# Optimization experiments

Measured on AMD Instinct MI355X. Metric: run time of the kernel, lower is better.

The kernel has to match this reference:

```python
import jax, jax.numpy as jnp
import numpy as np

N_EMBD = 1024
N_HEAD = 16
HEAD_DIM = N_EMBD // N_HEAD
SCALE = HEAD_DIM ** -0.5


def setup_inputs() -> dict:
    key = jax.random.key(0)
    ks = jax.random.split(key, 6)
    B, T = 64, 256
    s = N_EMBD ** -0.5
    return {
        "x": jax.random.normal(ks[0], (B, T, N_EMBD), dtype=jnp.float32),
        "Wq": jax.random.normal(ks[1], (N_EMBD, N_EMBD), dtype=jnp.float32) * s,
        "Wk": jax.random.normal(ks[2], (N_EMBD, N_EMBD), dtype=jnp.float32) * s,
        "Wv": jax.random.normal(ks[3], (N_EMBD, N_EMBD), dtype=jnp.float32) * s,
        "Wo": jax.random.normal(ks[4], (N_EMBD, N_EMBD), dtype=jnp.float32) * s,
        "bo": jax.random.normal(ks[5], (N_EMBD,), dtype=jnp.float32) * 0.01,
    }


def reference(x, Wq, Wk, Wv, Wo, bo):
    B, T, C = x.shape
    # QKV projections (no bias), split heads -> [B, H, T, Dh]
    def heads(y):
        return y.reshape(B, T, N_HEAD, HEAD_DIM).transpose(0, 2, 1, 3)
    q = heads(x @ Wq)
    k = heads(x @ Wk)
    v = heads(x @ Wv)
    # scaled causal attention scores [B, H, T, T]
    wei = jnp.einsum("bhqd,bhkd->bhqk", q, k) * SCALE
    causal = jnp.tril(jnp.ones((T, T), dtype=bool))
    wei = jnp.where(causal, wei, -jnp.inf)
    wei = jax.nn.softmax(wei, axis=-1)
    # dropout is identity in eval mode
    out = jnp.einsum("bhqk,bhkd->bhqd", wei, v)
    out = out.transpose(0, 2, 1, 3).reshape(B, T, C)
    return out @ Wo + bo
```

## Files before the change

kernel.cpp:

```cpp
#include <hip/hip_runtime.h>
#include <hip/hip_bf16.h>
#include <stdint.h>

typedef __attribute__((ext_vector_type(8))) short bfx8;
typedef __attribute__((ext_vector_type(4))) short bfx4;
typedef __attribute__((ext_vector_type(4))) float f32x4;
typedef __attribute__((ext_vector_type(4))) unsigned short us4;

#define SCALE_ATT 0.125f

__device__ __forceinline__ unsigned short f2bf(float f) {
  union { float f; unsigned u; } a; a.f = f;
  unsigned r = a.u + 0x7fffu + ((a.u >> 16) & 1u);
  return (unsigned short)(r >> 16);
}

__device__ __forceinline__ void gll16(const void* g, void* l) {
  __builtin_amdgcn_global_load_lds(
      (__attribute__((address_space(1))) void*)(g),
      (__attribute__((address_space(3))) void*)(l), 16, 0, 0);
}

__device__ __forceinline__ bfx8 ld2x64(const unsigned short* p) {
  bfx4 lo = *(const bfx4*)p;
  bfx4 hi = *(const bfx4*)(p + 4);
  return __builtin_shufflevector(lo, hi, 0, 1, 2, 3, 4, 5, 6, 7);
}

__global__ __launch_bounds__(256) void cvt_x(const float* __restrict__ x,
                                             unsigned short* __restrict__ xb, int n4) {
  int i = blockIdx.x * blockDim.x + threadIdx.x;
  int stride = gridDim.x * blockDim.x;
  const float4* x4 = (const float4*)x;
  for (; i < n4; i += stride) {
    float4 v = x4[i];
    us4 o;
    o[0] = f2bf(v.x); o[1] = f2bf(v.y); o[2] = f2bf(v.z); o[3] = f2bf(v.w);
    *(us4*)&xb[(size_t)i * 4] = o;
  }
}

__global__ __launch_bounds__(256) void cvt_w(const float* __restrict__ W0, const float* __restrict__ W1,
                                             const float* __restrict__ W2, const float* __restrict__ W3,
                                             unsigned short* __restrict__ T0, unsigned short* __restrict__ T1,
                                             unsigned short* __restrict__ T2, unsigned short* __restrict__ T3) {
  const float* W; unsigned short* T;
  switch (blockIdx.z) {
    case 0: W = W0; T = T0; break;
    case 1: W = W1; T = T1; break;
    case 2: W = W2; T = T2; break;
    default: W = W3; T = T3; break;
  }
  __shared__ unsigned short Ts[64][68];
  int k0 = blockIdx.x * 64, n0 = blockIdx.y * 64;
  int t = threadIdx.x;
  int lrow = t >> 4, c4 = t & 15;
  #pragma unroll
  for (int i = 0; i < 4; i++) {
    int row = lrow + i * 16;
    float4 v = *(const float4*)&W[(size_t)(k0 + row) * 1024 + n0 + c4 * 4];
    Ts[c4 * 4 + 0][row] = f2bf(v.x);
    Ts[c4 * 4 + 1][row] = f2bf(v.y);
    Ts[c4 * 4 + 2][row] = f2bf(v.z);
    Ts[c4 * 4 + 3][row] = f2bf(v.w);
  }
  __syncthreads();
  int f = t >> 5, sub = t & 31;
  int nt_l = f >> 1, ks_l = f & 1;
  size_t base = ((size_t)(((n0 >> 4) + nt_l) * 32 + (k0 >> 5) + ks_l)) * 512;
  #pragma unroll
  for (int i = 0; i < 2; i++) {
    int l = sub * 2 + i;
    int row = nt_l * 16 + (l & 15);
    int col = ks_l * 32 + ((l >> 4) << 3);
    us4 a = *(const us4*)&Ts[row][col];
    us4 b = *(const us4*)&Ts[row][col + 4];
    *(us4*)&T[base + l * 8] = a;
    *(us4*)&T[base + l * 8 + 4] = b;
  }
}

#define DS_BAR() __builtin_amdgcn_s_barrier()
#define SB0() __builtin_amdgcn_sched_barrier(0)
#define LGKM(N) do { asm volatile("s_waitcnt lgkmcnt(" #N ")" ::: "memory"); SB0(); } while (0)
#define VMW(N) do { asm volatile("s_waitcnt vmcnt(" #N ")" ::: "memory"); SB0(); } while (0)

#define STAGE(hs, gb, r0, kbyte) do { \
  const char* _g = (const char*)(gb) + (size_t)((r0) + srow) * 2048 + (size_t)(kbyte) + scolb; \
  gll16(_g, (hs) + w * 1024); \
  gll16(_g + 16 * 2048, (hs) + w * 1024 + 512); \
} while (0)

#define LOADA(dst, ptr, qm) \
  _Pragma("unroll") for (int mi = 0; mi < 4; ++mi) \
    dst[mi] = *(const bfx8*)&(ptr)[(wm * 128 + (qm) * 64 + mi * 16 + lr) * 32 + rcol];

#define LOADBG(dst, ks) \
  _Pragma("unroll") for (int ni = 0; ni < 4; ++ni) \
    dst[ni] = *(const bfx8*)&Bpw[((size_t)(ni * 32 + (ks))) * 512];

#define MFMA16(rb, a, b) \
  _Pragma("unroll") for (int mi = 0; mi < 4; ++mi) \
    _Pragma("unroll") for (int ni = 0; ni < 4; ++ni) \
      acc[(rb) + mi][ni] = __builtin_amdgcn_mfma_f32_16x16x32_bf16(a[mi], b[ni], acc[(rb) + mi][ni], 0, 0, 0);

template<int MODE>
__global__ __launch_bounds__(512, 2) void gemm8p(
    const unsigned short* __restrict__ A,
    const unsigned short* __restrict__ Bt0, const unsigned short* __restrict__ Bt1,
    const unsigned short* __restrict__ Bt2,
    unsigned short* __restrict__ O0, unsigned short* __restrict__ O1,
    unsigned short* __restrict__ O2,
    const float* __restrict__ bias, float* __restrict__ OutF, int nby) {
  __shared__ unsigned short A0s[2][256 * 32];
  __shared__ unsigned short A1s[2][256 * 32];

  int tid = threadIdx.x;
  int w = tid >> 6, l = tid & 63;
  int lr = l & 15, lh = l >> 4;
  int wm = w >> 2, wn = w & 3;
  int srow = w * 32 + (l >> 2);
  int scolb = ((l & 3) * 16) ^ (((l >> 5) & 1) << 5);
  int rcol = (lh * 8) ^ (((lr >> 3) & 1) << 4);

  int cpx = gridDim.x >> 3;
  int o = blockIdx.x;
  int wg = (o & 7) * cpx + (o >> 3);
  int bm = wg / nby, bn = wg % nby;

  const unsigned short* Bt;
  unsigned short* Ob = nullptr;
  int n0;
  if (MODE == 0) {
    int sel = bn >> 2;
    n0 = (bn & 3) * 256;
    Bt = sel == 0 ? Bt0 : (sel == 1 ? Bt1 : Bt2);
    Ob = sel == 0 ? O0 : (sel == 1 ? O1 : O2);
  } else {
    Bt = Bt0;
    n0 = bn * 256;
  }
  int am0 = bm * 256;
  const unsigned short* Bpw = Bt + ((size_t)((n0 >> 4) + wn * 4) * 32) * 512 + (size_t)l * 8;

  f32x4 acc[8][4];
  #pragma unroll
  for (int i = 0; i < 8; ++i)
    #pragma unroll
    for (int jj = 0; jj < 4; ++jj) acc[i][jj] = (f32x4){0.f, 0.f, 0.f, 0.f};

  bfx8 af[4], ag[4], b0[4], b1[4];

  STAGE(A0s[0], A, am0, 0);   STAGE(A1s[0], A, am0, 64);  SB0();
  LOADBG(b0, 0); SB0();
  LOADBG(b1, 1); SB0();
  VMW(8);
  DS_BAR();

  int cur = 0;
  #pragma unroll 1
  for (int t = 0; t < 15; ++t) {
    int kb = (t + 1) * 128;
    int ks2 = (t + 1) * 2;
    unsigned short* A0c = A0s[cur];       unsigned short* A1c = A1s[cur];
    unsigned short* A0n = A0s[cur ^ 1];   unsigned short* A1n = A1s[cur ^ 1];
    LOADA(af, A0c, 0);  LOADA(ag, A0c, 1);  SB0();
    STAGE(A0n, A, am0, kb);  STAGE(A1n, A, am0, kb + 64);  SB0();
    LGKM(4); VMW(8);
    __builtin_amdgcn_s_setprio(1);  MFMA16(0, af, b0);
    __builtin_amdgcn_s_setprio(0);
    LGKM(0);
    __builtin_amdgcn_s_setprio(1);  MFMA16(4, ag, b0);
    __builtin_amdgcn_s_setprio(0);
    LOADBG(b0, ks2); SB0();
    LOADA(af, A1c, 0);  LOADA(ag, A1c, 1);  SB0();
    LGKM(4); VMW(8);
    __builtin_amdgcn_s_setprio(1);  MFMA16(0, af, b1);
    __builtin_amdgcn_s_setprio(0);
    LGKM(0);
    __builtin_amdgcn_s_setprio(1);  MFMA16(4, ag, b1);
    __builtin_amdgcn_s_setprio(0);
    LOADBG(b1, ks2 + 1); SB0();
    VMW(8);
    DS_BAR();
    cur ^= 1;
  }
  LOADA(af, A0s[1], 0);  LOADA(ag, A0s[1], 1);  SB0();
  LGKM(4); VMW(4);
  __builtin_amdgcn_s_setprio(1);  MFMA16(0, af, b0);
  __builtin_amdgcn_s_setprio(0);
  LGKM(0);
  __builtin_amdgcn_s_setprio(1);  MFMA16(4, ag, b0);
  __builtin_amdgcn_s_setprio(0);
  LOADA(af, A1s[1], 0);  LOADA(ag, A1s[1], 1);  SB0();
  LGKM(4); VMW(0);
  __builtin_amdgcn_s_setprio(1);  MFMA16(0, af, b1);
  __builtin_amdgcn_s_setprio(0);
  LGKM(0);
  __builtin_amdgcn_s_setprio(1);  MFMA16(4, ag, b1);
  __builtin_amdgcn_s_setprio(0);

  float bv[4];
  if (MODE == 1) {
    #pragma unroll
    for (int ni = 0; ni < 4; ++ni) bv[ni] = bias[n0 + wn * 64 + ni * 16 + lr];
  }
  #pragma unroll
  for (int mi8 = 0; mi8 < 8; ++mi8)
    #pragma unroll
    for (int ni = 0; ni < 4; ++ni)
      #pragma unroll
      for (int j = 0; j < 4; ++j) {
        int r = am0 + wm * 128 + mi8 * 16 + lh * 4 + j;
        int c = n0 + wn * 64 + ni * 16 + lr;
        if (MODE == 0)
          Ob[(size_t)r * 1024 + c] = f2bf(acc[mi8][ni][j]);
        else
          OutF[(size_t)r * 1024 + c] = acc[mi8][ni][j] + bv[ni];
      }
}

__global__ __launch_bounds__(256, 4) void attn_kernel(
    const unsigned short* __restrict__ Qb, const unsigned short* __restrict__ Kb,
    const unsigned short* __restrict__ Vb, unsigned short* __restrict__ Ab) {
  __shared__ unsigned short Vt[64][260];
  __shared__ unsigned short Pw[4][16][36];

  int t = threadIdx.x;
  int w = t >> 6, l = t & 63;
  int lr = l & 15, lh = l >> 4;
  int bh = blockIdx.x;
  size_t rowbase = (size_t)(bh >> 4) * 256 * 1024 + (size_t)(bh & 15) * 64;

  {
    int rr = t >> 3, part = t & 7;
    for (int i = 0; i < 8; i++) {
      int row = i * 32 + rr;
      bfx8 vv = *(const bfx8*)(Vb + rowbase + (size_t)row * 1024 + part * 8);
      #pragma unroll
      for (int e = 0; e < 8; e++) Vt[part * 8 + e][row] = (unsigned short)vv[e];
    }
  }
  __syncthreads();

  for (int qt = 0; qt < 4; qt++) {
    int r0 = qt * 64 + w * 16;
    int rmax = r0 + 15;
    const unsigned short* Qrow = Qb + rowbase + (size_t)(r0 + lr) * 1024 + lh * 8;
    bfx8 aq0 = *(const bfx8*)(Qrow);
    bfx8 aq1 = *(const bfx8*)(Qrow + 32);

    float m[4], lsum[4];
    #pragma unroll
    for (int j = 0; j < 4; j++) { m[j] = -1e30f; lsum[j] = 0.f; }
    f32x4 oc[4];
    #pragma unroll
    for (int ct = 0; ct < 4; ct++) oc[ct] = (f32x4){0.f, 0.f, 0.f, 0.f};

    int nkc = (rmax >> 6) + 1;
    for (int kc = 0; kc < nkc; kc++) {
      int kbase = kc * 64;
      bool haveB = (kbase + 32) <= rmax;
      const unsigned short* Kr = Kb + rowbase + (size_t)(kbase + lr) * 1024 + lh * 8;

      bfx8 k0a = *(const bfx8*)(Kr);
      bfx8 k0b = *(const bfx8*)(Kr + 32);
      bfx8 k1a = *(const bfx8*)(Kr + 16 * 1024);
      bfx8 k1b = *(const bfx8*)(Kr + 16 * 1024 + 32);
      f32x4 s0 = (f32x4){0.f, 0.f, 0.f, 0.f};
      f32x4 s1 = (f32x4){0.f, 0.f, 0.f, 0.f};
      f32x4 s2 = (f32x4){0.f, 0.f, 0.f, 0.f};
      f32x4 s3 = (f32x4){0.f, 0.f, 0.f, 0.f};
      s0 = __builtin_amdgcn_mfma_f32_16x16x32_bf16(aq0, k0a, s0, 0, 0, 0);
      s0 = __builtin_amdgcn_mfma_f32_16x16x32_bf16(aq1, k0b, s0, 0, 0, 0);
      s1 = __builtin_amdgcn_mfma_f32_16x16x32_bf16(aq0, k1a, s1, 0, 0, 0);
      s1 = __builtin_amdgcn_mfma_f32_16x16x32_bf16(aq1, k1b, s1, 0, 0, 0);
      if (haveB) {
        bfx8 k2a = *(const bfx8*)(Kr + 32 * 1024);
        bfx8 k2b = *(const bfx8*)(Kr + 32 * 1024 + 32);
        bfx8 k3a = *(const bfx8*)(Kr + 48 * 1024);
        bfx8 k3b = *(const bfx8*)(Kr + 48 * 1024 + 32);
        s2 = __builtin_amdgcn_mfma_f32_16x16x32_bf16(aq0, k2a, s2, 0, 0, 0);
        s2 = __builtin_amdgcn_mfma_f32_16x16x32_bf16(aq1, k2b, s2, 0, 0, 0);
        s3 = __builtin_amdgcn_mfma_f32_16x16x32_bf16(aq0, k3a, s3, 0, 0, 0);
        s3 = __builtin_amdgcn_mfma_f32_16x16x32_bf16(aq1, k3b, s3, 0, 0, 0);
      }

      int c0 = kbase + lr, c1 = c0 + 16, c2 = c0 + 32, c3 = c0 + 48;
      unsigned pb[4];
      #pragma unroll
      for (int j = 0; j < 4; j++) {
        int row = r0 + lh * 4 + j;
        float v0 = (c0 <= row) ? s0[j] : -1e30f;
        float v1 = (c1 <= row) ? s1[j] : -1e30f;
        float v2 = (c2 <= row) ? s2[j] : -1e30f;
        float v3 = (c3 <= row) ? s3[j] : -1e30f;
        float cm = fmaxf(fmaxf(v0, v1), fmaxf(v2, v3));
        cm = fmaxf(cm, __shfl_xor(cm, 1));
        cm = fmaxf(cm, __shfl_xor(cm, 2));
        cm = fmaxf(cm, __shfl_xor(cm, 4));
        cm = fmaxf(cm, __shfl_xor(cm, 8));
        float mn = fmaxf(m[j], cm);
        float sc = __expf((m[j] - mn) * SCALE_ATT);
        float p0 = (c0 <= row) ? __expf((s0[j] - mn) * SCALE_ATT) : 0.f;
        float p1 = (c1 <= row) ? __expf((s1[j] - mn) * SCALE_ATT) : 0.f;
        float p2 = (c2 <= row) ? __expf((s2[j] - mn) * SCALE_ATT) : 0.f;
        float p3 = (c3 <= row) ? __expf((s3[j] - mn) * SCALE_ATT) : 0.f;
        m[j] = mn;
        float cs = (p0 + p1) + (p2 + p3);
        cs += __shfl_xor(cs, 1);
        cs += __shfl_xor(cs, 2);
        cs += __shfl_xor(cs, 4);
        cs += __shfl_xor(cs, 8);
        lsum[j] = lsum[j] * sc + cs;
        #pragma unroll
        for (int ct = 0; ct < 4; ct++) oc[ct][j] *= sc;
        Pw[w][lh * 4 + j][lr] = f2bf(p0);
        Pw[w][lh * 4 + j][16 + lr] = f2bf(p1);
        pb[j] = (unsigned)f2bf(p2) | ((unsigned)f2bf(p3) << 16);
      }

      {
        bfx8 pa = ld2x64(&Pw[w][lr][lh * 8]);
        #pragma unroll
        for (int ct = 0; ct < 4; ct++) {
          bfx8 vb = ld2x64(&Vt[ct * 16 + lr][kbase + lh * 8]);
          oc[ct] = __builtin_amdgcn_mfma_f32_16x16x32_bf16(pa, vb, oc[ct], 0, 0, 0);
        }
      }
      if (haveB) {
        #pragma unroll
        for (int j = 0; j < 4; j++) {
          Pw[w][lh * 4 + j][lr] = (unsigned short)(pb[j] & 0xffffu);
          Pw[w][lh * 4 + j][16 + lr] = (unsigned short)(pb[j] >> 16);
        }
        bfx8 pa = ld2x64(&Pw[w][lr][lh * 8]);
        #pragma unroll
        for (int ct = 0; ct < 4; ct++) {
          bfx8 vb = ld2x64(&Vt[ct * 16 + lr][kbase + 32 + lh * 8]);
          oc[ct] = __builtin_amdgcn_mfma_f32_16x16x32_bf16(pa, vb, oc[ct], 0, 0, 0);
        }
      }
    }

    float rinv[4];
    #pragma unroll
    for (int j = 0; j < 4; j++) rinv[j] = 1.0f / lsum[j];
    #pragma unroll
    for (int ct = 0; ct < 4; ct++)
      #pragma unroll
      for (int j = 0; j < 4; j++) {
        int row = r0 + lh * 4 + j;
        Ab[rowbase + (size_t)row * 1024 + ct * 16 + lr] = f2bf(oc[ct][j] * rinv[j]);
      }
  }
}

extern "C" void kernel_launch(void* const* d_in, const int* in_sizes, int n_in,
                              void* d_out, int out_size, void* d_ws, size_t ws_size,
                              hipStream_t stream) {
  const float* x  = (const float*)d_in[0];
  const float* Wq = (const float*)d_in[1];
  const float* Wk = (const float*)d_in[2];
  const float* Wv = (const float*)d_in[3];
  const float* Wo = (const float*)d_in[4];
  const float* bo = (const float*)d_in[5];
  float* out = (float*)d_out;

  char* ws = (char*)d_ws;
  unsigned short* xb  = (unsigned short*)(ws);
  unsigned short* Wtq = (unsigned short*)(ws + (size_t)(32u << 20));
  unsigned short* Wtk = (unsigned short*)(ws + (size_t)(34u << 20));
  unsigned short* Wtv = (unsigned short*)(ws + (size_t)(36u << 20));
  unsigned short* Wto = (unsigned short*)(ws + (size_t)(38u << 20));
  unsigned short* Qb  = (unsigned short*)(ws + (size_t)(40u << 20));
  unsigned short* Kb  = (unsigned short*)(ws + (size_t)(72u << 20));
  unsigned short* Vb  = (unsigned short*)(ws + (size_t)(104u << 20));
  unsigned short* Ab  = xb;

  cvt_x<<<2048, 256, 0, stream>>>(x, xb, 4194304);
  cvt_w<<<dim3(16, 16, 4), 256, 0, stream>>>(Wq, Wk, Wv, Wo, Wtq, Wtk, Wtv, Wto);
  gemm8p<0><<<768, 512, 0, stream>>>(xb, Wtq, Wtk, Wtv, Qb, Kb, Vb, nullptr, nullptr, 12);
  attn_kernel<<<1024, 256, 0, stream>>>(Qb, Kb, Vb, Ab);
  gemm8p<1><<<256, 512, 0, stream>>>(Ab, Wto, Wto, Wto, nullptr, nullptr, nullptr, bo, out, 4);
}
```

Baseline: 209.1 us.

## Switch projection GEMMs from 16x16x32 to 32x32x16 bf16 MFMA tiles

Rewrites the QKV and output projection GEMM inner loops to use 32x32x16 MFMA instructions instead of 16x16x32. The pre-transposed weight tile layout, the LDS A-fragment addressing and swizzle, the B fragment loads and the epilogue row/column mapping are all changed to match the 32x32 operand and accumulator layouts. The aim is fewer MFMA issues and fewer fragment loads per unit of work, with higher per-instruction throughput. It risks new LDS bank conflicts and requires the weight-transform kernel and GEMM layouts to agree exactly.

```diff
diff --git a/kernel.cpp b/kernel.cpp
--- a/kernel.cpp
+++ b/kernel.cpp
@@ -5,6 +5,7 @@
 typedef __attribute__((ext_vector_type(8))) short bfx8;
 typedef __attribute__((ext_vector_type(4))) short bfx4;
 typedef __attribute__((ext_vector_type(4))) float f32x4;
+typedef __attribute__((ext_vector_type(16))) float f32x16;
 typedef __attribute__((ext_vector_type(4))) unsigned short us4;
 
 #define SCALE_ATT 0.125f
@@ -66,13 +67,13 @@
   }
   __syncthreads();
   int f = t >> 5, sub = t & 31;
-  int nt_l = f >> 1, ks_l = f & 1;
-  size_t base = ((size_t)(((n0 >> 4) + nt_l) * 32 + (k0 >> 5) + ks_l)) * 512;
+  int nt_l = f >> 2, ks_l = f & 3;
+  size_t base = ((size_t)(((n0 >> 5) + nt_l) * 64 + (k0 >> 4) + ks_l)) * 512;
   #pragma unroll
   for (int i = 0; i < 2; i++) {
     int l = sub * 2 + i;
-    int row = nt_l * 16 + (l & 15);
-    int col = ks_l * 32 + ((l >> 4) << 3);
+    int row = nt_l * 32 + (l & 31);
+    int col = ks_l * 16 + ((l >> 5) << 3);
     us4 a = *(const us4*)&Ts[row][col];
     us4 b = *(const us4*)&Ts[row][col + 4];
     *(us4*)&T[base + l * 8] = a;
@@ -91,18 +92,22 @@
   gll16(_g + 16 * 2048, (hs) + w * 1024 + 512); \
 } while (0)
 
-#define LOADA(dst, ptr, qm) \
+#define LOADA32(dst, ptr, ksl) \
   _Pragma("unroll") for (int mi = 0; mi < 4; ++mi) \
-    dst[mi] = *(const bfx8*)&(ptr)[(wm * 128 + (qm) * 64 + mi * 16 + lr) * 32 + rcol];
-
-#define LOADBG(dst, ks) \
-  _Pragma("unroll") for (int ni = 0; ni < 4; ++ni) \
-    dst[ni] = *(const bfx8*)&Bpw[((size_t)(ni * 32 + (ks))) * 512];
-
-#define MFMA16(rb, a, b) \
-  _Pragma("unroll") for (int mi = 0; mi < 4; ++mi) \
-    _Pragma("unroll") for (int ni = 0; ni < 4; ++ni) \
-      acc[(rb) + mi][ni] = __builtin_amdgcn_mfma_f32_16x16x32_bf16(a[mi], b[ni], acc[(rb) + mi][ni], 0, 0, 0);
+    dst[mi] = *(const bfx8*)&(ptr)[(wm * 128 + mi * 32 + l31) * 32 + ((((ksl) << 4) + rcA) ^ rsw)];
+
+#define LOADBG32(dst, ks) do { \
+  dst[0] = *(const bfx8*)&Bpw[((size_t)(ks)) * 512]; \
+  dst[1] = *(const bfx8*)&Bpw[((size_t)(64 + (ks))) * 512]; \
+  dst[2] = *(const bfx8*)&Bpw[((size_t)((ks) + 1)) * 512]; \
+  dst[3] = *(const bfx8*)&Bpw[((size_t)(64 + (ks) + 1)) * 512]; \
+} while (0)
+
+#define MFMA8(a4, bA, bB) \
+  _Pragma("unroll") for (int mi = 0; mi < 4; ++mi) { \
+    acc[mi][0] = __builtin_amdgcn_mfma_f32_32x32x16_bf16(a4[mi], bA, acc[mi][0], 0, 0, 0); \
+    acc[mi][1] = __builtin_amdgcn_mfma_f32_32x32x16_bf16(a4[mi], bB, acc[mi][1], 0, 0, 0); \
+  }
 
 template<int MODE>
 __global__ __launch_bounds__(512, 2) void gemm8p(
@@ -117,11 +122,12 @@
 
   int tid = threadIdx.x;
   int w = tid >> 6, l = tid & 63;
-  int lr = l & 15, lh = l >> 4;
+  int l31 = l & 31, lhi = l >> 5;
   int wm = w >> 2, wn = w & 3;
   int srow = w * 32 + (l >> 2);
   int scolb = ((l & 3) * 16) ^ (((l >> 5) & 1) << 5);
-  int rcol = (lh * 8) ^ (((lr >> 3) & 1) << 4);
+  int rcA = lhi << 3;
+  int rsw = ((l >> 3) & 1) << 4;
 
   int cpx = gridDim.x >> 3;
   int o = blockIdx.x;
@@ -141,19 +147,21 @@
     n0 = bn * 256;
   }
   int am0 = bm * 256;
-  const unsigned short* Bpw = Bt + ((size_t)((n0 >> 4) + wn * 4) * 32) * 512 + (size_t)l * 8;
-
-  f32x4 acc[8][4];
+  const unsigned short* Bpw = Bt + ((size_t)((n0 >> 5) + wn * 2) * 64) * 512 + (size_t)l * 8;
+
+  f32x16 acc[4][2];
   #pragma unroll
-  for (int i = 0; i < 8; ++i)
-    #pragma unroll
-    for (int jj = 0; jj < 4; ++jj) acc[i][jj] = (f32x4){0.f, 0.f, 0.f, 0.f};
+  for (int i = 0; i < 4; ++i)
+    #pragma unroll
+    for (int jj = 0; jj < 2; ++jj)
+      #pragma unroll
+      for (int e = 0; e < 16; ++e) acc[i][jj][e] = 0.f;
 
   bfx8 af[4], ag[4], b0[4], b1[4];
 
   STAGE(A0s[0], A, am0, 0);   STAGE(A1s[0], A, am0, 64);  SB0();
-  LOADBG(b0, 0); SB0();
-  LOADBG(b1, 1); SB0();
+  LOADBG32(b0, 0); SB0();
+  LOADBG32(b1, 2); SB0();
   VMW(8);
   DS_BAR();
 
@@ -161,62 +169,62 @@
   #pragma unroll 1
   for (int t = 0; t < 15; ++t) {
     int kb = (t + 1) * 128;
-    int ks2 = (t + 1) * 2;
+    int ksn = (t + 1) * 4;
     unsigned short* A0c = A0s[cur];       unsigned short* A1c = A1s[cur];
     unsigned short* A0n = A0s[cur ^ 1];   unsigned short* A1n = A1s[cur ^ 1];
-    LOADA(af, A0c, 0);  LOADA(ag, A0c, 1);  SB0();
+    LOADA32(af, A0c, 0);  LOADA32(ag, A0c, 1);  SB0();
     STAGE(A0n, A, am0, kb);  STAGE(A1n, A, am0, kb + 64);  SB0();
     LGKM(4); VMW(8);
-    __builtin_amdgcn_s_setprio(1);  MFMA16(0, af, b0);
+    __builtin_amdgcn_s_setprio(1);  MFMA8(af, b0[0], b0[1]);
     __builtin_amdgcn_s_setprio(0);
     LGKM(0);
-    __builtin_amdgcn_s_setprio(1);  MFMA16(4, ag, b0);
+    __builtin_amdgcn_s_setprio(1);  MFMA8(ag, b0[2], b0[3]);
     __builtin_amdgcn_s_setprio(0);
-    LOADBG(b0, ks2); SB0();
-    LOADA(af, A1c, 0);  LOADA(ag, A1c, 1);  SB0();
+    LOADBG32(b0, ksn); SB0();
+    LOADA32(af, A1c, 0);  LOADA32(ag, A1c, 1);  SB0();
     LGKM(4); VMW(8);
-    __builtin_amdgcn_s_setprio(1);  MFMA16(0, af, b1);
+    __builtin_amdgcn_s_setprio(1);  MFMA8(af, b1[0], b1[1]);
     __builtin_amdgcn_s_setprio(0);
     LGKM(0);
-    __builtin_amdgcn_s_setprio(1);  MFMA16(4, ag, b1);
+    __builtin_amdgcn_s_setprio(1);  MFMA8(ag, b1[2], b1[3]);
     __builtin_amdgcn_s_setprio(0);
-    LOADBG(b1, ks2 + 1); SB0();
+    LOADBG32(b1, ksn + 2); SB0();
     VMW(8);
     DS_BAR();
     cur ^= 1;
   }
-  LOADA(af, A0s[1], 0);  LOADA(ag, A0s[1], 1);  SB0();
+  LOADA32(af, A0s[1], 0);  LOADA32(ag, A0s[1], 1);  SB0();
   LGKM(4); VMW(4);
-  __builtin_amdgcn_s_setprio(1);  MFMA16(0, af, b0);
+  __builtin_amdgcn_s_setprio(1);  MFMA8(af, b0[0], b0[1]);
   __builtin_amdgcn_s_setprio(0);
   LGKM(0);
-  __builtin_amdgcn_s_setprio(1);  MFMA16(4, ag, b0);
+  __builtin_amdgcn_s_setprio(1);  MFMA8(ag, b0[2], b0[3]);
   __builtin_amdgcn_s_setprio(0);
-  LOADA(af, A1s[1], 0);  LOADA(ag, A1s[1], 1);  SB0();
+  LOADA32(af, A1s[1], 0);  LOADA32(ag, A1s[1], 1);  SB0();
   LGKM(4); VMW(0);
-  __builtin_amdgcn_s_setprio(1);  MFMA16(0, af, b1);
+  __builtin_amdgcn_s_setprio(1);  MFMA8(af, b1[0], b1[1]);
   __builtin_amdgcn_s_setprio(0);
   LGKM(0);
-  __builtin_amdgcn_s_setprio(1);  MFMA16(4, ag, b1);
+  __builtin_amdgcn_s_setprio(1);  MFMA8(ag, b1[2], b1[3]);
   __builtin_amdgcn_s_setprio(0);
 
-  float bv[4];
+  float bv[2];
   if (MODE == 1) {
     #pragma unroll
-    for (int ni = 0; ni < 4; ++ni) bv[ni] = bias[n0 + wn * 64 + ni * 16 + lr];
+    for (int ni = 0; ni < 2; ++ni) bv[ni] = bias[n0 + wn * 64 + ni * 32 + l31];
   }
   #pragma unroll
-  for (int mi8 = 0; mi8 < 8; ++mi8)
-    #pragma unroll
-    for (int ni = 0; ni < 4; ++ni)
-      #pragma unroll
-      for (int j = 0; j < 4; ++j) {
-        int r = am0 + wm * 128 + mi8 * 16 + lh * 4 + j;
-        int c = n0 + wn * 64 + ni * 16 + lr;
+  for (int mi = 0; mi < 4; ++mi)
+    #pragma unroll
+    for (int ni = 0; ni < 2; ++ni)
+      #pragma unroll
+      for (int reg = 0; reg < 16; ++reg) {
+        int r = am0 + wm * 128 + mi * 32 + (reg & 3) + 8 * (reg >> 2) + 4 * lhi;
+        int c = n0 + wn * 64 + ni * 32 + l31;
         if (MODE == 0)
-          Ob[(size_t)r * 1024 + c] = f2bf(acc[mi8][ni][j]);
+          Ob[(size_t)r * 1024 + c] = f2bf(acc[mi][ni][reg]);
         else
-          OutF[(size_t)r * 1024 + c] = acc[mi8][ni][j] + bv[ni];
+          OutF[(size_t)r * 1024 + c] = acc[mi][ni][reg] + bv[ni];
       }
 }
 
```

Result: slower. 244.7 us (+17.0%).
